# Optimization experiments

Hardware: AMD Instinct MI355X
Metric: run time of the kernel (lower is better)

The kernel has to match this reference:

```python
import jax, jax.numpy as jnp
import numpy as np

B, S, HID, H = 8, 128, 256, 4
DH = HID // H
FF = 4 * HID


def setup_inputs() -> dict:
    key = jax.random.key(0)
    ks = jax.random.split(key, 16)
    n = lambda i, shape: jax.random.normal(ks[i], shape, dtype=jnp.float32) * 0.02
    z = lambda shape: jnp.zeros(shape, dtype=jnp.float32)
    return dict(
        x=jax.random.normal(ks[0], (B, S, HID), dtype=jnp.float32),
        attention_mask=jnp.zeros((B, 1, S, S), dtype=jnp.float32),
        Wq=n(1, (HID, HID)), bq=z((HID,)),
        Wk=n(2, (HID, HID)), bk=z((HID,)),
        Wv=n(3, (HID, HID)), bv=z((HID,)),
        order_w=n(4, (2 * DH,)), order_b=z(()),
        dist_w=n(5, (2 * DH,)), dist_b=z(()),
        scalar=jax.random.normal(ks[6], (1,), dtype=jnp.float32),
        AWq=n(7, (HID, HID)), Abq=z((HID,)),
        AWk=n(8, (HID, HID)), Abk=z((HID,)),
        Wd=n(9, (HID, HID)), bd=z((HID,)),
        g1=jnp.ones((HID,), jnp.float32), beta1=z((HID,)),
        W1=n(10, (HID, FF)), b1=z((FF,)),
        W2=n(11, (FF, HID)), b2=z((HID,)),
        g2=jnp.ones((HID,), jnp.float32), beta2=z((HID,)),
    )


def _ln(t, g, b, eps=1e-12):
    m = t.mean(-1, keepdims=True)
    v = ((t - m) ** 2).mean(-1, keepdims=True)
    return (t - m) / jnp.sqrt(v + eps) * g + b


def _heads(t):
    # [B,S,HID] -> [B,H,S,DH]
    return t.reshape(B, S, H, DH).transpose(0, 2, 1, 3)


def reference(x, attention_mask, Wq, bq, Wk, bk, Wv, bv, order_w, order_b,
              dist_w, dist_b, scalar, AWq, Abq, AWk, Abk, Wd, bd,
              g1, beta1, W1, b1, W2, b2, g2, beta2):
    inv = 1.0 / jnp.sqrt(jnp.float32(DH))
    q = x @ Wq + bq
    k = x @ Wk + bk
    v = x @ Wv + bv
    qh, kh, vh = _heads(q), _heads(k), _heads(v)
    scores = jnp.einsum('bhqd,bhkd->bhqk', qh, kh)  # [B,H,S,S]

    # order/distance affines on concat(q_i, k_j): Linear(2*DH,1) decomposes into
    # per-token projections summed via broadcast (same math, no [B,H,S,S,2*DH] tensor)
    pr_order = jax.nn.sigmoid((qh @ order_w[:DH])[..., :, None]
                              + (kh @ order_w[DH:])[..., None, :] + order_b)
    gd_order = jnp.triu(jnp.ones((S, S), jnp.float32), k=1)
    err_order = (jnp.log(pr_order + 1e-24) * gd_order
                 + jnp.log(1.0 - pr_order + 1e-24) * (1.0 - gd_order))

    idx = jnp.arange(S)
    gd_dist = jnp.log(jnp.abs(idx[None, :] - idx[:, None]).astype(jnp.float32) + 1.0)
    pr_dist = ((qh @ dist_w[:DH])[..., :, None]
               + (kh @ dist_w[DH:])[..., None, :] + dist_b)
    err_dist = -jnp.square(gd_dist - pr_dist) * jnp.square(scalar[0]) * 0.5

    rich_scores = scores + err_order + err_dist
    softm = lambda s: jax.nn.softmax(s * inv + attention_mask, axis=-1)
    rich_probs = softm(rich_scores)
    origin_probs = softm(scores)

    # rich/calibrated combine ('fixed'): softmax(origin + 0.5 * rich)
    combined = jax.nn.softmax(origin_probs + 0.5 * rich_probs, axis=-1)

    # two-level attack attention on transformed mixed q/k
    aq, ak = _heads(q @ AWq + Abq), _heads(k @ AWk + Abk)
    attack_probs = softm(jnp.einsum('bhqd,bhkd->bhqk', aq, ak))
    final_probs = jax.nn.softmax(combined + 0.5 * attack_probs, axis=-1)

    ctx = jnp.einsum('bhqk,bhkd->bhqd', final_probs, vh)
    ctx = ctx.transpose(0, 2, 1, 3).reshape(B, S, HID)
    h = _ln(ctx @ Wd + bd + x, g1, beta1)
    f = jax.nn.gelu(h @ W1 + b1, approximate=False) @ W2 + b2
    return _ln(f + h, g2, beta2)
```

## Files before the change

### kernel.cpp

```cpp
#include <hip/hip_runtime.h>
#include <hip/hip_bf16.h>
#include <math.h>

#define B_  8
#define S_  128
#define HID_ 256
#define H_  4
#define DH_ 64
#define FF_ 1024
#define M_  (B_ * S_)

typedef _Float16 half_t;
typedef __attribute__((ext_vector_type(8))) _Float16 half8;
typedef __attribute__((ext_vector_type(4))) float floatx4;

enum { EP_F32 = 0, EP_F16 = 1, EP_F16B = 2, EP_GELU = 3, EP_PROJ = 4 };

__device__ __forceinline__ floatx4 mfma16(half8 a, half8 b, floatx4 c) {
    return __builtin_amdgcn_mfma_f32_16x16x32_f16(a, b, c, 0, 0, 0);
}

__device__ __forceinline__ float wred_sum(float v) {
#pragma unroll
    for (int o = 32; o >= 1; o >>= 1) v += __shfl_xor(v, o, 64);
    return v;
}
__device__ __forceinline__ float block_sum_256(float v, float* s4, int tid) {
    v = wred_sum(v);
    __syncthreads();
    if ((tid & 63) == 0) s4[tid >> 6] = v;
    __syncthreads();
    return s4[0] + s4[1] + s4[2] + s4[3];
}
__device__ __forceinline__ float qred_sum(float v) {
#pragma unroll
    for (int o = 1; o < 16; o <<= 1) v += __shfl_xor(v, o, 64);
    return v;
}
__device__ __forceinline__ void sm8(float (&v)[8]) {
    float s = 0.f;
#pragma unroll
    for (int j = 0; j < 8; ++j) { v[j] = __expf(v[j]); s += v[j]; }
    s = qred_sum(s);
    float r = 1.f / s;
#pragma unroll
    for (int j = 0; j < 8; ++j) v[j] *= r;
}

template<int EPI>
__device__ __forceinline__ void mgemm(
    const half_t* __restrict__ A, int ldA,
    const half_t* __restrict__ Bt, int ldB,
    int kLen, int m0, int n0,
    const float* __restrict__ bias,
    float* __restrict__ Cf, half_t* __restrict__ Ch, int ldC,
    const float* __restrict__ pw1, const float* __restrict__ pw2,
    float* __restrict__ po1, float* __restrict__ po2, int hsel)
{
    __shared__ half8 Asf[2][4][64];
    __shared__ half8 Bsf[2][4][64];

    const int tid = threadIdx.x;
    const int w = tid >> 6, l = tid & 63;
    const int sr = tid >> 2;
    const int sq = tid & 3;
    const int sdst = (sr & 15) | (sq << 4);
    const int smt = sr >> 4;
    const half_t* Ap = A + (size_t)(m0 + sr) * ldA + sq * 8;
    const half_t* Bp = Bt + (size_t)(n0 + sr) * ldB + sq * 8;

    half8 ra, rb;
    auto fetch = [&](int t) {
        ra = *(const half8*)(Ap + t * 32);
        rb = *(const half8*)(Bp + t * 32);
    };
    auto commit = [&](int buf) {
        Asf[buf][smt][sdst] = ra;
        Bsf[buf][smt][sdst] = rb;
    };

    floatx4 zero = {0.f, 0.f, 0.f, 0.f};
    floatx4 acc[4] = {zero, zero, zero, zero};
    const int kt = kLen >> 5;

    fetch(0);
    commit(0);
    __syncthreads();
    for (int t = 0; t < kt; ++t) {
        const bool more = (t + 1 < kt);
        if (more) fetch(t + 1);
        const int buf = t & 1;
        half8 a = Asf[buf][w][l];
        acc[0] = mfma16(a, Bsf[buf][0][l], acc[0]);
        acc[1] = mfma16(a, Bsf[buf][1][l], acc[1]);
        acc[2] = mfma16(a, Bsf[buf][2][l], acc[2]);
        acc[3] = mfma16(a, Bsf[buf][3][l], acc[3]);
        if (more) {
            commit((t + 1) & 1);
            __syncthreads();
        }
    }

    const int quad = l >> 4, lc = l & 15;
    const int rowb = m0 + w * 16 + quad * 4;
    float bvv[4] = {0.f, 0.f, 0.f, 0.f};
    if (EPI >= EP_F16B) {
#pragma unroll
        for (int nt = 0; nt < 4; ++nt) bvv[nt] = bias[n0 + nt * 16 + lc];
    }
    float pw1v[4], pw2v[4];
    if (EPI == EP_PROJ) {
#pragma unroll
        for (int nt = 0; nt < 4; ++nt) {
            pw1v[nt] = pw1[nt * 16 + lc];
            pw2v[nt] = pw2[nt * 16 + lc];
        }
    }
#pragma unroll
    for (int rr = 0; rr < 4; ++rr) {
        float ov[4];
#pragma unroll
        for (int nt = 0; nt < 4; ++nt) {
            float o = acc[nt][rr];
            if (EPI >= EP_F16B) o += bvv[nt];
            if (EPI == EP_GELU) o = 0.5f * o * (1.f + erff(o * 0.70710678118654752f));
            ov[nt] = o;
            const size_t ci = (size_t)(rowb + rr) * ldC + n0 + nt * 16 + lc;
            if (EPI == EP_F32) Cf[ci] = o;
            else Ch[ci] = (half_t)o;
        }
        if (EPI == EP_PROJ) {
            float po = ov[0] * pw1v[0] + ov[1] * pw1v[1] + ov[2] * pw1v[2] + ov[3] * pw1v[3];
            float pd = ov[0] * pw2v[0] + ov[1] * pw2v[1] + ov[2] * pw2v[2] + ov[3] * pw2v[3];
#pragma unroll
            for (int off = 1; off < 16; off <<= 1) {
                po += __shfl_xor(po, off, 64);
                pd += __shfl_xor(pd, off, 64);
            }
            if (lc == 0) {
                const int m = rowb + rr;
                const int idx = ((m >> 7) * H_ + hsel) * S_ + (m & 127);
                po1[idx] = po;
                po2[idx] = pd;
            }
        }
    }
}

__global__ __launch_bounds__(256) void prep_kernel(
    const float* __restrict__ x,
    const float* __restrict__ Wq, const float* __restrict__ Wk,
    const float* __restrict__ Wv, const float* __restrict__ Wd,
    const float* __restrict__ AWq, const float* __restrict__ AWk,
    const float* __restrict__ W1, const float* __restrict__ W2,
    half_t* __restrict__ x16, half_t* __restrict__ Wq16n, half_t* __restrict__ Wk16n,
    half_t* __restrict__ WqT, half_t* __restrict__ WkT, half_t* __restrict__ WvT,
    half_t* __restrict__ WdT, half_t* __restrict__ AWqT, half_t* __restrict__ AWkT,
    half_t* __restrict__ W1T, half_t* __restrict__ W2T)
{
    const int z = blockIdx.z, bx = blockIdx.x, by = blockIdx.y;
    const int tid = threadIdx.x;
    if (z < 3) {
        const float* src = (z == 0) ? x : (z == 1) ? Wq : Wk;
        half_t* dst = (z == 0) ? x16 : (z == 1) ? Wq16n : Wk16n;
        const int total = (z == 0) ? M_ * HID_ : HID_ * HID_;
        const int bid = by * 16 + bx;
        if (bid * 1024 < total) {
            const int base = bid * 1024 + tid * 4;
            float4 vv = *(const float4*)(src + base);
            dst[base + 0] = (half_t)vv.x;
            dst[base + 1] = (half_t)vv.y;
            dst[base + 2] = (half_t)vv.z;
            dst[base + 3] = (half_t)vv.w;
        }
        return;
    }
    const float* src; half_t* dst; int K, N, k0, n0;
    if (z <= 8) {
        const float* ins[6] = {Wq, Wk, Wv, Wd, AWq, AWk};
        half_t* outs[6] = {WqT, WkT, WvT, WdT, AWqT, AWkT};
        src = ins[z - 3]; dst = outs[z - 3];
        K = 256; N = 256; k0 = bx * 64; n0 = by * 64;
        if (bx >= 4 || by >= 4) return;
    } else if (z == 9) {
        src = W1; dst = W1T; K = 256; N = 1024;
        k0 = bx * 64; n0 = by * 64;
        if (bx >= 4) return;
    } else {
        src = W2; dst = W2T; K = 1024; N = 256;
        k0 = by * 64; n0 = bx * 64;
        if (bx >= 4) return;
    }
    __shared__ half_t tl[64][72];
    const int r = tid >> 2, c0 = (tid & 3) * 16;
#pragma unroll 4
    for (int i = 0; i < 16; ++i)
        tl[c0 + i][r] = (half_t)src[(size_t)(k0 + r) * N + n0 + c0 + i];
    __syncthreads();
#pragma unroll 4
    for (int i = 0; i < 16; ++i)
        dst[(size_t)(n0 + r) * K + k0 + c0 + i] = tl[r][c0 + i];
}

__global__ __launch_bounds__(256) void compose_mfma(
    const half_t* __restrict__ AWqT, const half_t* __restrict__ AWkT,
    const half_t* __restrict__ Wq16n, const half_t* __restrict__ Wk16n,
    const float* __restrict__ AWq, const float* __restrict__ AWk,
    const float* __restrict__ bq, const float* __restrict__ bk,
    const float* __restrict__ Abq, const float* __restrict__ Abk,
    half_t* __restrict__ WcqT, half_t* __restrict__ WckT,
    float* __restrict__ bcq, float* __restrict__ bck)
{
    const int z = blockIdx.z;
    if (blockIdx.y < 4) {
        const half_t* A = z ? AWkT : AWqT;
        const half_t* Bt = z ? Wk16n : Wq16n;
        half_t* C = z ? WckT : WcqT;
        mgemm<EP_F16>(A, HID_, Bt, HID_, HID_, blockIdx.y * 64, blockIdx.x * 64,
                      nullptr, nullptr, C, HID_, nullptr, nullptr, nullptr, nullptr, 0);
    } else {
        __shared__ float red[4][64];
        const float* bsrc = z ? bk : bq;
        const float* AW   = z ? AWk : AWq;
        const float* Ab   = z ? Abk : Abq;
        float* bco        = z ? bck : bcq;
        int t = threadIdx.x, l = t & 63, kc = t >> 6;
        int n = blockIdx.x * 64 + l;
        float p = 0.f;
#pragma unroll 8
        for (int kk = 0; kk < 64; ++kk) {
            int k = kc * 64 + kk;
            p = fmaf(bsrc[k], AW[(size_t)k * HID_ + n], p);
        }
        red[kc][l] = p;
        __syncthreads();
        if (kc == 0)
            bco[n] = red[0][l] + red[1][l] + red[2][l] + red[3][l] + Ab[n];
    }
}

__global__ __launch_bounds__(256) void xgemm5(
    const half_t* __restrict__ x16,
    const half_t* __restrict__ WqT, const float* __restrict__ bq,
    const half_t* __restrict__ WkT, const float* __restrict__ bk,
    const half_t* __restrict__ WvT, const float* __restrict__ bv,
    const half_t* __restrict__ WcqT, const float* __restrict__ bcq,
    const half_t* __restrict__ WckT, const float* __restrict__ bck,
    const float* __restrict__ order_w, const float* __restrict__ dist_w,
    half_t* __restrict__ q16, half_t* __restrict__ k16, half_t* __restrict__ v16,
    half_t* __restrict__ aq16, half_t* __restrict__ ak16,
    float* __restrict__ qoA, float* __restrict__ qdA,
    float* __restrict__ koA, float* __restrict__ kdA)
{
    const int z = blockIdx.z;
    const int m0 = blockIdx.y * 64, n0 = blockIdx.x * 64;
    if (z == 0)
        mgemm<EP_PROJ>(x16, HID_, WqT, HID_, HID_, m0, n0, bq, nullptr, q16, HID_,
                       order_w, dist_w, qoA, qdA, blockIdx.x);
    else if (z == 1)
        mgemm<EP_PROJ>(x16, HID_, WkT, HID_, HID_, m0, n0, bk, nullptr, k16, HID_,
                       order_w + DH_, dist_w + DH_, koA, kdA, blockIdx.x);
    else if (z == 2)
        mgemm<EP_F16B>(x16, HID_, WvT, HID_, HID_, m0, n0, bv, nullptr, v16, HID_,
                       nullptr, nullptr, nullptr, nullptr, 0);
    else if (z == 3)
        mgemm<EP_F16B>(x16, HID_, WcqT, HID_, HID_, m0, n0, bcq, nullptr, aq16, HID_,
                       nullptr, nullptr, nullptr, nullptr, 0);
    else
        mgemm<EP_F16B>(x16, HID_, WckT, HID_, HID_, m0, n0, bck, nullptr, ak16, HID_,
                       nullptr, nullptr, nullptr, nullptr, 0);
}

__global__ __launch_bounds__(64) void attn_fused(
    const half_t* __restrict__ q16, const half_t* __restrict__ k16,
    const half_t* __restrict__ v16, const half_t* __restrict__ aq16,
    const half_t* __restrict__ ak16,
    const float* __restrict__ qoA, const float* __restrict__ qdA,
    const float* __restrict__ koA, const float* __restrict__ kdA,
    const float* __restrict__ mask,
    const float* __restrict__ order_b_p, const float* __restrict__ dist_b_p,
    const float* __restrict__ scalar_p,
    half_t* __restrict__ ctx16)
{
    __shared__ half8 Qf[2][64], AQf[2][64];
    __shared__ half8 Kf[2][8][64], AKf[2][8][64];
    __shared__ half_t Vt[64][136];
    __shared__ half_t Pm[16][136];

    const int l = threadIdx.x;
    const int quad = l >> 4, lc = l & 15;
    const int bh = blockIdx.x >> 3, rt = blockIdx.x & 7;
    const int b = bh >> 2, h = bh & 3;
    const size_t hoff = (size_t)b * S_ * HID_ + h * DH_;

#pragma unroll
    for (int u = 0; u < 2; ++u) {
        int idx = u * 64 + l;
        int r = idx >> 3, c = idx & 7;
        size_t g = hoff + (size_t)(rt * 16 + r) * HID_ + c * 8;
        int kt = c >> 2, sl = r | ((c & 3) << 4);
        Qf[kt][sl]  = *(const half8*)(q16 + g);
        AQf[kt][sl] = *(const half8*)(aq16 + g);
    }
#pragma unroll
    for (int u = 0; u < 16; ++u) {
        int idx = u * 64 + l;
        int j = idx >> 3, c = idx & 7;
        size_t g = hoff + (size_t)j * HID_ + c * 8;
        int kt = c >> 2, jt = j >> 4, sl = (j & 15) | ((c & 3) << 4);
        Kf[kt][jt][sl]  = *(const half8*)(k16 + g);
        AKf[kt][jt][sl] = *(const half8*)(ak16 + g);
    }
#pragma unroll
    for (int u = 0; u < 16; ++u) {
        int j = (u >> 3) * 64 + l;
        int c = u & 7;
        half8 vv = *(const half8*)(v16 + hoff + (size_t)j * HID_ + c * 8);
#pragma unroll
        for (int e = 0; e < 8; ++e) Vt[c * 8 + e][j] = vv[e];
    }
    __syncthreads();

    floatx4 zero = {0.f, 0.f, 0.f, 0.f};
    floatx4 accS[8], accA[8];
#pragma unroll
    for (int jt = 0; jt < 8; ++jt) { accS[jt] = zero; accA[jt] = zero; }
#pragma unroll
    for (int kt = 0; kt < 2; ++kt) {
        half8 a0 = Qf[kt][l];
        half8 a1 = AQf[kt][l];
#pragma unroll
        for (int jt = 0; jt < 8; ++jt) {
            accS[jt] = mfma16(a0, Kf[kt][jt][l], accS[jt]);
            accA[jt] = mfma16(a1, AKf[kt][jt][l], accA[jt]);
        }
    }

    const float ob = order_b_p[0], db = dist_b_p[0];
    const float scl = scalar_p[0];
    const float s2 = scl * scl;
    const float inv = 0.125f;
    float kov[8], kdv[8];
#pragma unroll
    for (int jt = 0; jt < 8; ++jt) {
        kov[jt] = koA[bh * S_ + jt * 16 + lc];
        kdv[jt] = kdA[bh * S_ + jt * 16 + lc];
    }
#pragma unroll
    for (int reg = 0; reg < 4; ++reg) {
        const int il = quad * 4 + reg;
        const int i  = rt * 16 + il;
        float qo = qoA[bh * S_ + i], qd = qdA[bh * S_ + i];
        const float* mrow = mask + ((size_t)(b * S_ + i)) * S_;
        float mk[8], lg[8], as_[8];
#pragma unroll
        for (int jt = 0; jt < 8; ++jt) {
            mk[jt] = mrow[jt * 16 + lc];
            lg[jt] = accS[jt][reg];
            as_[jt] = accA[jt][reg];
        }
        float p0[8];
#pragma unroll
        for (int jt = 0; jt < 8; ++jt) p0[jt] = lg[jt] * inv + mk[jt];
        sm8(p0);
        float p1[8];
#pragma unroll
        for (int jt = 0; jt < 8; ++jt) {
            int j = jt * 16 + lc;
            float pr = 1.f / (1.f + __expf(-(qo + kov[jt] + ob)));
            float sel = (j > i) ? pr : 1.f - pr;
            float erro = __logf(sel + 1e-24f);
            float gd = __logf(fabsf((float)(j - i)) + 1.f);
            float dd = gd - (qd + kdv[jt] + db);
            p1[jt] = (lg[jt] + erro - 0.5f * dd * dd * s2) * inv + mk[jt];
        }
        sm8(p1);
#pragma unroll
        for (int jt = 0; jt < 8; ++jt) p0[jt] += 0.5f * p1[jt];
        sm8(p0);
#pragma unroll
        for (int jt = 0; jt < 8; ++jt) p1[jt] = as_[jt] * inv + mk[jt];
        sm8(p1);
#pragma unroll
        for (int jt = 0; jt < 8; ++jt) p0[jt] += 0.5f * p1[jt];
        sm8(p0);
#pragma unroll
        for (int jt = 0; jt < 8; ++jt) Pm[il][jt * 16 + lc] = (half_t)p0[jt];
    }
    __syncthreads();

    half8 pa_[4];
#pragma unroll
    for (int kt = 0; kt < 4; ++kt)
        pa_[kt] = *(const half8*)&Pm[lc][kt * 32 + quad * 8];
    floatx4 apv[4];
#pragma unroll
    for (int nt = 0; nt < 4; ++nt) apv[nt] = zero;
#pragma unroll
    for (int nt = 0; nt < 4; ++nt) {
#pragma unroll
        for (int kt = 0; kt < 4; ++kt) {
            half8 vf = *(const half8*)&Vt[nt * 16 + lc][kt * 32 + quad * 8];
            apv[nt] = mfma16(pa_[kt], vf, apv[nt]);
        }
    }
#pragma unroll
    for (int nt = 0; nt < 4; ++nt) {
#pragma unroll
        for (int reg = 0; reg < 4; ++reg) {
            int i = rt * 16 + quad * 4 + reg;
            ctx16[hoff + (size_t)i * HID_ + nt * 16 + lc] = (half_t)apv[nt][reg];
        }
    }
}

__global__ __launch_bounds__(256) void dense_mfma(
    const half_t* __restrict__ ctx16, const half_t* __restrict__ WdT,
    float* __restrict__ dn)
{
    mgemm<EP_F32>(ctx16, HID_, WdT, HID_, HID_, blockIdx.y * 64, blockIdx.x * 64,
                  nullptr, dn, nullptr, HID_, nullptr, nullptr, nullptr, nullptr, 0);
}

__global__ __launch_bounds__(256) void ff1_mfma(
    const half_t* __restrict__ h16, const half_t* __restrict__ W1T,
    const float* __restrict__ b1, half_t* __restrict__ f116)
{
    mgemm<EP_GELU>(h16, HID_, W1T, HID_, HID_, blockIdx.y * 64, blockIdx.x * 64,
                   b1, nullptr, f116, FF_, nullptr, nullptr, nullptr, nullptr, 0);
}

__global__ __launch_bounds__(256) void ff2_mfma(
    const half_t* __restrict__ f116, const half_t* __restrict__ W2T,
    float* __restrict__ p0, float* __restrict__ p1,
    float* __restrict__ p2, float* __restrict__ p3)
{
    const int z = blockIdx.z;
    float* C = (z == 0) ? p0 : (z == 1) ? p1 : (z == 2) ? p2 : p3;
    mgemm<EP_F32>(f116 + z * 256, FF_, W2T + z * 256, FF_, 256,
                  blockIdx.y * 64, blockIdx.x * 64,
                  nullptr, C, nullptr, HID_, nullptr, nullptr, nullptr, nullptr, 0);
}

__global__ __launch_bounds__(256) void ln1_kernel(
    const float* __restrict__ dn, const float* __restrict__ bd,
    const float* __restrict__ x,
    const float* __restrict__ g1, const float* __restrict__ beta1,
    float* __restrict__ h32, half_t* __restrict__ h16)
{
    __shared__ float s4[4];
    const int row = blockIdx.x;
    const int n = threadIdx.x;
    const size_t idx = (size_t)row * HID_ + n;
    float val = dn[idx] + bd[n] + x[idx];
    float mean = block_sum_256(val, s4, n) * (1.f / HID_);
    float dv = val - mean;
    float var = block_sum_256(dv * dv, s4, n) * (1.f / HID_);
    float r = dv * rsqrtf(var + 1e-12f) * g1[n] + beta1[n];
    h32[idx] = r;
    h16[idx] = (half_t)r;
}

__global__ __launch_bounds__(256) void ln2_kernel(
    const float* __restrict__ p0, const float* __restrict__ p1,
    const float* __restrict__ p2, const float* __restrict__ p3,
    const float* __restrict__ b2, const float* __restrict__ h32,
    const float* __restrict__ g2, const float* __restrict__ beta2,
    float* __restrict__ out)
{
    __shared__ float s4[4];
    const int row = blockIdx.x;
    const int n = threadIdx.x;
    const size_t idx = (size_t)row * HID_ + n;
    float val = p0[idx] + p1[idx] + p2[idx] + p3[idx] + b2[n] + h32[idx];
    float mean = block_sum_256(val, s4, n) * (1.f / HID_);
    float dv = val - mean;
    float var = block_sum_256(dv * dv, s4, n) * (1.f / HID_);
    out[idx] = dv * rsqrtf(var + 1e-12f) * g2[n] + beta2[n];
}

extern "C" void kernel_launch(void* const* d_in, const int* in_sizes, int n_in,
                              void* d_out, int out_size, void* d_ws, size_t ws_size,
                              hipStream_t stream) {
    const float* x        = (const float*)d_in[0];
    const float* mask     = (const float*)d_in[1];
    const float* Wq       = (const float*)d_in[2];
    const float* bq       = (const float*)d_in[3];
    const float* Wk       = (const float*)d_in[4];
    const float* bk       = (const float*)d_in[5];
    const float* Wv       = (const float*)d_in[6];
    const float* bv       = (const float*)d_in[7];
    const float* order_w  = (const float*)d_in[8];
    const float* order_b  = (const float*)d_in[9];
    const float* dist_w   = (const float*)d_in[10];
    const float* dist_b   = (const float*)d_in[11];
    const float* scalar   = (const float*)d_in[12];
    const float* AWq      = (const float*)d_in[13];
    const float* Abq      = (const float*)d_in[14];
    const float* AWk      = (const float*)d_in[15];
    const float* Abk      = (const float*)d_in[16];
    const float* Wd       = (const float*)d_in[17];
    const float* bd       = (const float*)d_in[18];
    const float* g1       = (const float*)d_in[19];
    const float* beta1    = (const float*)d_in[20];
    const float* W1       = (const float*)d_in[21];
    const float* b1       = (const float*)d_in[22];
    const float* W2       = (const float*)d_in[23];
    const float* b2       = (const float*)d_in[24];
    const float* g2       = (const float*)d_in[25];
    const float* beta2    = (const float*)d_in[26];

    float* ws = (float*)d_ws;
    size_t off = 0;
    auto afl = [&](size_t n) { float* p = ws + off; off += n; return p; };
    auto ahf = [&](size_t nh) { half_t* p = (half_t*)(ws + off); off += nh / 2; return p; };

    half_t* x16   = ahf(M_ * HID_);
    half_t* Wq16n = ahf(HID_ * HID_);
    half_t* Wk16n = ahf(HID_ * HID_);
    half_t* WqT   = ahf(HID_ * HID_);
    half_t* WkT   = ahf(HID_ * HID_);
    half_t* WvT   = ahf(HID_ * HID_);
    half_t* WdT   = ahf(HID_ * HID_);
    half_t* AWqT  = ahf(HID_ * HID_);
    half_t* AWkT  = ahf(HID_ * HID_);
    half_t* W1T   = ahf(HID_ * FF_);
    half_t* W2T   = ahf(HID_ * FF_);
    half_t* WcqT  = ahf(HID_ * HID_);
    half_t* WckT  = ahf(HID_ * HID_);
    half_t* q16   = ahf(M_ * HID_);
    half_t* k16   = ahf(M_ * HID_);
    half_t* v16   = ahf(M_ * HID_);
    half_t* aq16  = ahf(M_ * HID_);
    half_t* ak16  = ahf(M_ * HID_);
    half_t* ctx16 = ahf(M_ * HID_);
    half_t* h16   = ahf(M_ * HID_);
    half_t* f116  = ahf(M_ * FF_);
    float* dnb  = afl(M_ * HID_);
    float* hb32 = afl(M_ * HID_);
    float* pf0  = afl(M_ * HID_);
    float* pf1  = afl(M_ * HID_);
    float* pf2  = afl(M_ * HID_);
    float* pf3  = afl(M_ * HID_);
    float* bcq  = afl(256);
    float* bck  = afl(256);
    float* qoA  = afl(B_ * H_ * S_);
    float* qdA  = afl(B_ * H_ * S_);
    float* koA  = afl(B_ * H_ * S_);
    float* kdA  = afl(B_ * H_ * S_);

    prep_kernel<<<dim3(16, 16, 11), 256, 0, stream>>>(
        x, Wq, Wk, Wv, Wd, AWq, AWk, W1, W2,
        x16, Wq16n, Wk16n, WqT, WkT, WvT, WdT, AWqT, AWkT, W1T, W2T);
    compose_mfma<<<dim3(4, 5, 2), 256, 0, stream>>>(
        AWqT, AWkT, Wq16n, Wk16n, AWq, AWk, bq, bk, Abq, Abk, WcqT, WckT, bcq, bck);
    xgemm5<<<dim3(4, 16, 5), 256, 0, stream>>>(
        x16, WqT, bq, WkT, bk, WvT, bv, WcqT, bcq, WckT, bck, order_w, dist_w,
        q16, k16, v16, aq16, ak16, qoA, qdA, koA, kdA);
    attn_fused<<<256, 64, 0, stream>>>(
        q16, k16, v16, aq16, ak16, qoA, qdA, koA, kdA,
        mask, order_b, dist_b, scalar, ctx16);
    dense_mfma<<<dim3(4, 16), 256, 0, stream>>>(ctx16, WdT, dnb);
    ln1_kernel<<<M_, 256, 0, stream>>>(dnb, bd, x, g1, beta1, hb32, h16);
    ff1_mfma<<<dim3(16, 16), 256, 0, stream>>>(h16, W1T, b1, f116);
    ff2_mfma<<<dim3(4, 16, 4), 256, 0, stream>>>(f116, W2T, pf0, pf1, pf2, pf3);
    ln2_kernel<<<M_, 256, 0, stream>>>(pf0, pf1, pf2, pf3, b2, hb32, g2, beta2, (float*)d_out);
}
```

Before: 162.7 us.

## Fuse all stages into one cooperative persistent kernel with grid syncs

Replaces the chain of nine kernel launches with a single cooperative kernel of 256 blocks that runs each stage as jobs separated by grid-wide barriers. It also fuses the dense projection with LayerNorm1, and FF2 with LayerNorm2, using 16-row tiles, which removes the split-K partial buffers and the separate LN kernels. The aim is to remove launch overhead and inter-kernel gaps on a small, latency-bound workload. The cost is grid-sync overhead, a larger shared-memory union that may limit occupancy, and fewer active blocks in the fused dense and FF2 stages. The old multi-kernel path is kept as a fallback if the cooperative launch fails.

New measurement: 390.7 us. 140% more time.

```diff
diff --git a/kernel.cpp b/kernel.cpp
--- a/kernel.cpp
+++ b/kernel.cpp
@@ -1,6 +1,8 @@
 #include <hip/hip_runtime.h>
-#include <hip/hip_bf16.h>
+#include <hip/hip_cooperative_groups.h>
 #include <math.h>
+
+namespace cg = cooperative_groups;
 
 #define B_  8
 #define S_  128
@@ -49,6 +51,7 @@
 
 template<int EPI>
 __device__ __forceinline__ void mgemm(
+    half8 (&Asf)[2][4][64], half8 (&Bsf)[2][4][64],
     const half_t* __restrict__ A, int ldA,
     const half_t* __restrict__ Bt, int ldB,
     int kLen, int m0, int n0,
@@ -57,9 +60,6 @@
     const float* __restrict__ pw1, const float* __restrict__ pw2,
     float* __restrict__ po1, float* __restrict__ po2, int hsel)
 {
-    __shared__ half8 Asf[2][4][64];
-    __shared__ half8 Bsf[2][4][64];
-
     const int tid = threadIdx.x;
     const int w = tid >> 6, l = tid & 63;
     const int sr = tid >> 2;
@@ -146,6 +146,374 @@
         }
     }
 }
+
+
+struct MegaParams {
+    const float *x, *mask, *Wq, *bq, *Wk, *bk, *Wv, *bv;
+    const float *order_w, *order_b, *dist_w, *dist_b, *scalar;
+    const float *AWq, *Abq, *AWk, *Abk, *Wd, *bd, *g1, *beta1;
+    const float *W1, *b1, *W2, *b2, *g2, *beta2;
+    half_t *x16, *Wq16n, *Wk16n, *WqT, *WkT, *WvT, *WdT, *AWqT, *AWkT, *W1T, *W2T;
+    half_t *WcqT, *WckT;
+    half_t *q16, *k16, *v16, *aq16, *ak16, *ctx16, *h16, *f116;
+    float *hb32, *bcq, *bck, *qoA, *qdA, *koA, *kdA;
+    float *out;
+};
+
+union SMem {
+    struct { half8 Asf[2][4][64]; half8 Bsf[2][4][64]; } g;
+    struct { half_t tl[64][72]; } p;
+    struct { float red[4][64]; } r;
+    struct {
+        half8 Kf[2][8][64]; half8 AKf[2][8][64];
+        half_t Vt[64][136]; half_t Pm[16][136];
+    } a;
+    struct { half8 Af[8][64]; float hS[16][257]; } d;
+    struct { half8 Af2[32][64]; float hS[16][257]; } f;
+};
+
+#define NJOBS_PREP 608
+__device__ __forceinline__ void prep_job(const MegaParams& P, SMem& sm, int j, int tid) {
+    if (j < 384) {
+        const float* src; half_t* dst; int base;
+        if (j < 256)      { src = P.x;  dst = P.x16;   base = j * 1024; }
+        else if (j < 320) { src = P.Wq; dst = P.Wq16n; base = (j - 256) * 1024; }
+        else              { src = P.Wk; dst = P.Wk16n; base = (j - 320) * 1024; }
+        float4 vv = *(const float4*)(src + base + tid * 4);
+        dst[base + tid * 4 + 0] = (half_t)vv.x;
+        dst[base + tid * 4 + 1] = (half_t)vv.y;
+        dst[base + tid * 4 + 2] = (half_t)vv.z;
+        dst[base + tid * 4 + 3] = (half_t)vv.w;
+        return;
+    }
+    int t = j - 384;
+    const float* src; half_t* dst; int K, N, k0, n0;
+    if (t < 96) {
+        int m = t >> 4, q = t & 15;
+        const float* ins[6] = {P.Wq, P.Wk, P.Wv, P.Wd, P.AWq, P.AWk};
+        half_t* outs[6] = {P.WqT, P.WkT, P.WvT, P.WdT, P.AWqT, P.AWkT};
+        src = ins[m]; dst = outs[m]; K = 256; N = 256;
+        k0 = (q & 3) * 64; n0 = (q >> 2) * 64;
+    } else if (t < 160) {
+        int q = t - 96; src = P.W1; dst = P.W1T; K = 256; N = 1024;
+        k0 = (q & 3) * 64; n0 = (q >> 2) * 64;
+    } else {
+        int q = t - 160; src = P.W2; dst = P.W2T; K = 1024; N = 256;
+        k0 = (q >> 2) * 64; n0 = (q & 3) * 64;
+    }
+    __syncthreads();
+    const int r = tid >> 2, c0 = (tid & 3) * 16;
+#pragma unroll 4
+    for (int i = 0; i < 16; ++i)
+        sm.p.tl[c0 + i][r] = (half_t)src[(size_t)(k0 + r) * N + n0 + c0 + i];
+    __syncthreads();
+#pragma unroll 4
+    for (int i = 0; i < 16; ++i)
+        dst[(size_t)(n0 + r) * K + k0 + c0 + i] = sm.p.tl[r][c0 + i];
+}
+
+__device__ __forceinline__ void compose_job(const MegaParams& P, SMem& sm, int blk, int tid) {
+    if (blk < 32) {
+        int z = blk >> 4, q = blk & 15;
+        const half_t* A  = z ? P.AWkT : P.AWqT;
+        const half_t* Bt = z ? P.Wk16n : P.Wq16n;
+        half_t* C = z ? P.WckT : P.WcqT;
+        mgemm<EP_F16>(sm.g.Asf, sm.g.Bsf, A, HID_, Bt, HID_, HID_,
+                      (q >> 2) * 64, (q & 3) * 64,
+                      nullptr, nullptr, C, HID_, nullptr, nullptr, nullptr, nullptr, 0);
+    } else {
+        int q = blk - 32;
+        int z = q >> 2, xb = q & 3;
+        const float* bsrc = z ? P.bk : P.bq;
+        const float* AW   = z ? P.AWk : P.AWq;
+        const float* Ab   = z ? P.Abk : P.Abq;
+        float* bco        = z ? P.bck : P.bcq;
+        int l = tid & 63, kc = tid >> 6;
+        int n = xb * 64 + l;
+        float p = 0.f;
+#pragma unroll 8
+        for (int kk = 0; kk < 64; ++kk) {
+            int k = kc * 64 + kk;
+            p = fmaf(bsrc[k], AW[(size_t)k * HID_ + n], p);
+        }
+        sm.r.red[kc][l] = p;
+        __syncthreads();
+        if (kc == 0)
+            bco[n] = sm.r.red[0][l] + sm.r.red[1][l] + sm.r.red[2][l] + sm.r.red[3][l] + Ab[n];
+    }
+}
+
+__device__ __forceinline__ void xgemm_job(const MegaParams& P, SMem& sm, int j) {
+    const int z = j >> 6, q = j & 63;
+    const int m0 = (q >> 2) * 64, n0 = (q & 3) * 64, bx = q & 3;
+    if (z == 0)
+        mgemm<EP_PROJ>(sm.g.Asf, sm.g.Bsf, P.x16, HID_, P.WqT, HID_, HID_, m0, n0,
+                       P.bq, nullptr, P.q16, HID_, P.order_w, P.dist_w, P.qoA, P.qdA, bx);
+    else if (z == 1)
+        mgemm<EP_PROJ>(sm.g.Asf, sm.g.Bsf, P.x16, HID_, P.WkT, HID_, HID_, m0, n0,
+                       P.bk, nullptr, P.k16, HID_, P.order_w + DH_, P.dist_w + DH_, P.koA, P.kdA, bx);
+    else if (z == 2)
+        mgemm<EP_F16B>(sm.g.Asf, sm.g.Bsf, P.x16, HID_, P.WvT, HID_, HID_, m0, n0,
+                       P.bv, nullptr, P.v16, HID_, nullptr, nullptr, nullptr, nullptr, 0);
+    else if (z == 3)
+        mgemm<EP_F16B>(sm.g.Asf, sm.g.Bsf, P.x16, HID_, P.WcqT, HID_, HID_, m0, n0,
+                       P.bcq, nullptr, P.aq16, HID_, nullptr, nullptr, nullptr, nullptr, 0);
+    else
+        mgemm<EP_F16B>(sm.g.Asf, sm.g.Bsf, P.x16, HID_, P.WckT, HID_, HID_, m0, n0,
+                       P.bck, nullptr, P.ak16, HID_, nullptr, nullptr, nullptr, nullptr, 0);
+}
+
+__device__ __forceinline__ void attn_job(const MegaParams& P, SMem& sm, int blk, int tid) {
+    const int bh = blk >> 3, rt = blk & 7;
+    const int b = bh >> 2, h = bh & 3;
+    const size_t hoff = (size_t)b * S_ * HID_ + (size_t)h * DH_;
+    const int l = tid & 63, w = tid >> 6;
+    const int quad = l >> 4, lc = l & 15;
+
+#pragma unroll
+    for (int u = 0; u < 4; ++u) {
+        int idx = u * 256 + tid;
+        int j = idx >> 3, c = idx & 7;
+        size_t g = hoff + (size_t)j * HID_ + c * 8;
+        int kt = c >> 2, jt = j >> 4, sl = (j & 15) | ((c & 3) << 4);
+        sm.a.Kf[kt][jt][sl]  = *(const half8*)(P.k16 + g);
+        sm.a.AKf[kt][jt][sl] = *(const half8*)(P.ak16 + g);
+    }
+#pragma unroll
+    for (int u = 0; u < 4; ++u) {
+        int idx = u * 256 + tid;
+        int j = idx >> 3, c = idx & 7;
+        half8 vv = *(const half8*)(P.v16 + hoff + (size_t)j * HID_ + c * 8);
+#pragma unroll
+        for (int e = 0; e < 8; ++e) sm.a.Vt[c * 8 + e][j] = vv[e];
+    }
+    __syncthreads();
+
+    if (w == 0) {
+        half8 qf[2], aqf[2];
+#pragma unroll
+        for (int kt = 0; kt < 2; ++kt) {
+            size_t g = hoff + (size_t)(rt * 16 + lc) * HID_ + kt * 32 + quad * 8;
+            qf[kt]  = *(const half8*)(P.q16 + g);
+            aqf[kt] = *(const half8*)(P.aq16 + g);
+        }
+        floatx4 zero = {0.f, 0.f, 0.f, 0.f};
+        floatx4 accS[8], accA[8];
+#pragma unroll
+        for (int jt = 0; jt < 8; ++jt) { accS[jt] = zero; accA[jt] = zero; }
+#pragma unroll
+        for (int kt = 0; kt < 2; ++kt) {
+#pragma unroll
+            for (int jt = 0; jt < 8; ++jt) {
+                accS[jt] = mfma16(qf[kt], sm.a.Kf[kt][jt][l], accS[jt]);
+                accA[jt] = mfma16(aqf[kt], sm.a.AKf[kt][jt][l], accA[jt]);
+            }
+        }
+
+        const float ob = P.order_b[0], db = P.dist_b[0];
+        const float scl = P.scalar[0];
+        const float s2 = scl * scl;
+        const float inv = 0.125f;
+        float kov[8], kdv[8];
+#pragma unroll
+        for (int jt = 0; jt < 8; ++jt) {
+            kov[jt] = P.koA[bh * S_ + jt * 16 + lc];
+            kdv[jt] = P.kdA[bh * S_ + jt * 16 + lc];
+        }
+#pragma unroll
+        for (int reg = 0; reg < 4; ++reg) {
+            const int il = quad * 4 + reg;
+            const int i  = rt * 16 + il;
+            float qo = P.qoA[bh * S_ + i], qd = P.qdA[bh * S_ + i];
+            const float* mrow = P.mask + ((size_t)(b * S_ + i)) * S_;
+            float mk[8], lg[8], as_[8];
+#pragma unroll
+            for (int jt = 0; jt < 8; ++jt) {
+                mk[jt] = mrow[jt * 16 + lc];
+                lg[jt] = accS[jt][reg];
+                as_[jt] = accA[jt][reg];
+            }
+            float p0[8];
+#pragma unroll
+            for (int jt = 0; jt < 8; ++jt) p0[jt] = lg[jt] * inv + mk[jt];
+            sm8(p0);
+            float p1[8];
+#pragma unroll
+            for (int jt = 0; jt < 8; ++jt) {
+                int j = jt * 16 + lc;
+                float pr = 1.f / (1.f + __expf(-(qo + kov[jt] + ob)));
+                float sel = (j > i) ? pr : 1.f - pr;
+                float erro = __logf(sel + 1e-24f);
+                float gd = __logf(fabsf((float)(j - i)) + 1.f);
+                float dd = gd - (qd + kdv[jt] + db);
+                p1[jt] = (lg[jt] + erro - 0.5f * dd * dd * s2) * inv + mk[jt];
+            }
+            sm8(p1);
+#pragma unroll
+            for (int jt = 0; jt < 8; ++jt) p0[jt] += 0.5f * p1[jt];
+            sm8(p0);
+#pragma unroll
+            for (int jt = 0; jt < 8; ++jt) p1[jt] = as_[jt] * inv + mk[jt];
+            sm8(p1);
+#pragma unroll
+            for (int jt = 0; jt < 8; ++jt) p0[jt] += 0.5f * p1[jt];
+            sm8(p0);
+#pragma unroll
+            for (int jt = 0; jt < 8; ++jt) sm.a.Pm[il][jt * 16 + lc] = (half_t)p0[jt];
+        }
+    }
+    __syncthreads();
+
+    if (w == 0) {
+        half8 pa_[4];
+#pragma unroll
+        for (int kt = 0; kt < 4; ++kt)
+            pa_[kt] = *(const half8*)&sm.a.Pm[lc][kt * 32 + quad * 8];
+        floatx4 zero = {0.f, 0.f, 0.f, 0.f};
+        floatx4 apv[4] = {zero, zero, zero, zero};
+#pragma unroll
+        for (int nt = 0; nt < 4; ++nt) {
+#pragma unroll
+            for (int kt = 0; kt < 4; ++kt) {
+                half8 vf = *(const half8*)&sm.a.Vt[nt * 16 + lc][kt * 32 + quad * 8];
+                apv[nt] = mfma16(pa_[kt], vf, apv[nt]);
+            }
+        }
+#pragma unroll
+        for (int nt = 0; nt < 4; ++nt) {
+#pragma unroll
+            for (int reg = 0; reg < 4; ++reg) {
+                int i = rt * 16 + quad * 4 + reg;
+                P.ctx16[hoff + (size_t)i * HID_ + nt * 16 + lc] = (half_t)apv[nt][reg];
+            }
+        }
+    }
+}
+
+template<bool DUAL>
+__device__ __forceinline__ void ln16(float (&hS)[16][257], int tid, int r0,
+    const float* __restrict__ g, const float* __restrict__ be,
+    float* __restrict__ o32, half_t* __restrict__ o16, float* __restrict__ oo) {
+    const int row = tid >> 4, jj = tid & 15;
+    float s = 0.f;
+#pragma unroll
+    for (int i = 0; i < 16; ++i) s += hS[row][i * 16 + jj];
+#pragma unroll
+    for (int o = 1; o < 16; o <<= 1) s += __shfl_xor(s, o, 64);
+    const float mean = s * (1.f / 256.f);
+    float vs = 0.f;
+#pragma unroll
+    for (int i = 0; i < 16; ++i) { float d = hS[row][i * 16 + jj] - mean; vs += d * d; }
+#pragma unroll
+    for (int o = 1; o < 16; o <<= 1) vs += __shfl_xor(vs, o, 64);
+    const float rs = rsqrtf(vs * (1.f / 256.f) + 1e-12f);
+#pragma unroll
+    for (int i = 0; i < 16; ++i) {
+        int col = i * 16 + jj;
+        float v = (hS[row][col] - mean) * rs * g[col] + be[col];
+        size_t gi = (size_t)(r0 + row) * HID_ + col;
+        if (DUAL) { o32[gi] = v; o16[gi] = (half_t)v; }
+        else      { oo[gi] = v; }
+    }
+}
+
+__device__ __forceinline__ void dense_ln1_job(const MegaParams& P, SMem& sm, int blk, int tid) {
+    const int r0 = blk * 16;
+#pragma unroll
+    for (int u = 0; u < 2; ++u) {
+        int idx = u * 256 + tid;
+        int row = idx >> 5, c = idx & 31;
+        sm.d.Af[c >> 2][row | ((c & 3) << 4)] =
+            *(const half8*)(P.ctx16 + (size_t)(r0 + row) * HID_ + c * 8);
+    }
+    __syncthreads();
+    const int w = tid >> 6, l = tid & 63;
+    const int n0 = w * 64, quad = l >> 4, lc = l & 15;
+    floatx4 zero = {0.f, 0.f, 0.f, 0.f};
+    floatx4 acc[4] = {zero, zero, zero, zero};
+#pragma unroll
+    for (int kt = 0; kt < 8; ++kt) {
+        half8 a = sm.d.Af[kt][l];
+#pragma unroll
+        for (int nt = 0; nt < 4; ++nt) {
+            half8 b = *(const half8*)(P.WdT + (size_t)(n0 + nt * 16 + lc) * HID_ + kt * 32 + quad * 8);
+            acc[nt] = mfma16(a, b, acc[nt]);
+        }
+    }
+#pragma unroll
+    for (int nt = 0; nt < 4; ++nt) {
+#pragma unroll
+        for (int rr = 0; rr < 4; ++rr) {
+            int row = quad * 4 + rr, col = n0 + nt * 16 + lc;
+            sm.d.hS[row][col] = acc[nt][rr] + P.bd[col] + P.x[(size_t)(r0 + row) * HID_ + col];
+        }
+    }
+    __syncthreads();
+    ln16<true>(sm.d.hS, tid, r0, P.g1, P.beta1, P.hb32, P.h16, nullptr);
+}
+
+__device__ __forceinline__ void ff1_job(const MegaParams& P, SMem& sm, int blk) {
+    mgemm<EP_GELU>(sm.g.Asf, sm.g.Bsf, P.h16, HID_, P.W1T, HID_, HID_,
+                   (blk >> 4) * 64, (blk & 15) * 64,
+                   P.b1, nullptr, P.f116, FF_, nullptr, nullptr, nullptr, nullptr, 0);
+}
+
+__device__ __forceinline__ void ff2_ln2_job(const MegaParams& P, SMem& sm, int blk, int tid) {
+    const int r0 = blk * 16;
+#pragma unroll
+    for (int u = 0; u < 8; ++u) {
+        int idx = u * 256 + tid;
+        int row = idx >> 7, c = idx & 127;
+        sm.f.Af2[c >> 2][row | ((c & 3) << 4)] =
+            *(const half8*)(P.f116 + (size_t)(r0 + row) * FF_ + c * 8);
+    }
+    __syncthreads();
+    const int w = tid >> 6, l = tid & 63;
+    const int n0 = w * 64, quad = l >> 4, lc = l & 15;
+    floatx4 zero = {0.f, 0.f, 0.f, 0.f};
+    floatx4 acc[4] = {zero, zero, zero, zero};
+#pragma unroll
+    for (int kt = 0; kt < 32; ++kt) {
+        half8 a = sm.f.Af2[kt][l];
+#pragma unroll
+        for (int nt = 0; nt < 4; ++nt) {
+            half8 b = *(const half8*)(P.W2T + (size_t)(n0 + nt * 16 + lc) * FF_ + kt * 32 + quad * 8);
+            acc[nt] = mfma16(a, b, acc[nt]);
+        }
+    }
+#pragma unroll
+    for (int nt = 0; nt < 4; ++nt) {
+#pragma unroll
+        for (int rr = 0; rr < 4; ++rr) {
+            int row = quad * 4 + rr, col = n0 + nt * 16 + lc;
+            sm.f.hS[row][col] = acc[nt][rr] + P.b2[col] + P.hb32[(size_t)(r0 + row) * HID_ + col];
+        }
+    }
+    __syncthreads();
+    ln16<false>(sm.f.hS, tid, r0, P.g2, P.beta2, nullptr, nullptr, P.out);
+}
+
+__global__ __launch_bounds__(256) void mega_kernel(MegaParams P) {
+    cg::grid_group gg = cg::this_grid();
+    __shared__ SMem sm;
+    const int blk = blockIdx.x, tid = threadIdx.x;
+
+    for (int j = blk; j < NJOBS_PREP; j += 256) prep_job(P, sm, j, tid);
+    __syncthreads(); gg.sync();
+    if (blk < 40) compose_job(P, sm, blk, tid);
+    __syncthreads(); gg.sync();
+    xgemm_job(P, sm, blk);
+    if (blk < 64) { __syncthreads(); xgemm_job(P, sm, blk + 256); }
+    __syncthreads(); gg.sync();
+    attn_job(P, sm, blk, tid);
+    __syncthreads(); gg.sync();
+    if (blk < 64) dense_ln1_job(P, sm, blk, tid);
+    __syncthreads(); gg.sync();
+    ff1_job(P, sm, blk);
+    __syncthreads(); gg.sync();
+    if (blk < 64) ff2_ln2_job(P, sm, blk, tid);
+}
+
 
 __global__ __launch_bounds__(256) void prep_kernel(
     const float* __restrict__ x,
@@ -211,12 +579,13 @@
     half_t* __restrict__ WcqT, half_t* __restrict__ WckT,
     float* __restrict__ bcq, float* __restrict__ bck)
 {
+    __shared__ half8 As[2][4][64], Bs[2][4][64];
     const int z = blockIdx.z;
     if (blockIdx.y < 4) {
         const half_t* A = z ? AWkT : AWqT;
         const half_t* Bt = z ? Wk16n : Wq16n;
         half_t* C = z ? WckT : WcqT;
-        mgemm<EP_F16>(A, HID_, Bt, HID_, HID_, blockIdx.y * 64, blockIdx.x * 64,
+        mgemm<EP_F16>(As, Bs, A, HID_, Bt, HID_, HID_, blockIdx.y * 64, blockIdx.x * 64,
                       nullptr, nullptr, C, HID_, nullptr, nullptr, nullptr, nullptr, 0);
     } else {
         __shared__ float red[4][64];
@@ -252,22 +621,23 @@
     float* __restrict__ qoA, float* __restrict__ qdA,
     float* __restrict__ koA, float* __restrict__ kdA)
 {
+    __shared__ half8 As[2][4][64], Bs[2][4][64];
     const int z = blockIdx.z;
     const int m0 = blockIdx.y * 64, n0 = blockIdx.x * 64;
     if (z == 0)
-        mgemm<EP_PROJ>(x16, HID_, WqT, HID_, HID_, m0, n0, bq, nullptr, q16, HID_,
+        mgemm<EP_PROJ>(As, Bs, x16, HID_, WqT, HID_, HID_, m0, n0, bq, nullptr, q16, HID_,
                        order_w, dist_w, qoA, qdA, blockIdx.x);
     else if (z == 1)
-        mgemm<EP_PROJ>(x16, HID_, WkT, HID_, HID_, m0, n0, bk, nullptr, k16, HID_,
+        mgemm<EP_PROJ>(As, Bs, x16, HID_, WkT, HID_, HID_, m0, n0, bk, nullptr, k16, HID_,
                        order_w + DH_, dist_w + DH_, koA, kdA, blockIdx.x);
     else if (z == 2)
-        mgemm<EP_F16B>(x16, HID_, WvT, HID_, HID_, m0, n0, bv, nullptr, v16, HID_,
+        mgemm<EP_F16B>(As, Bs, x16, HID_, WvT, HID_, HID_, m0, n0, bv, nullptr, v16, HID_,
                        nullptr, nullptr, nullptr, nullptr, 0);
     else if (z == 3)
-        mgemm<EP_F16B>(x16, HID_, WcqT, HID_, HID_, m0, n0, bcq, nullptr, aq16, HID_,
+        mgemm<EP_F16B>(As, Bs, x16, HID_, WcqT, HID_, HID_, m0, n0, bcq, nullptr, aq16, HID_,
                        nullptr, nullptr, nullptr, nullptr, 0);
     else
-        mgemm<EP_F16B>(x16, HID_, WckT, HID_, HID_, m0, n0, bck, nullptr, ak16, HID_,
+        mgemm<EP_F16B>(As, Bs, x16, HID_, WckT, HID_, HID_, m0, n0, bck, nullptr, ak16, HID_,
                        nullptr, nullptr, nullptr, nullptr, 0);
 }
 
@@ -418,7 +788,8 @@
     const half_t* __restrict__ ctx16, const half_t* __restrict__ WdT,
     float* __restrict__ dn)
 {
-    mgemm<EP_F32>(ctx16, HID_, WdT, HID_, HID_, blockIdx.y * 64, blockIdx.x * 64,
+    __shared__ half8 As[2][4][64], Bs[2][4][64];
+    mgemm<EP_F32>(As, Bs, ctx16, HID_, WdT, HID_, HID_, blockIdx.y * 64, blockIdx.x * 64,
                   nullptr, dn, nullptr, HID_, nullptr, nullptr, nullptr, nullptr, 0);
 }
 
@@ -426,7 +797,8 @@
     const half_t* __restrict__ h16, const half_t* __restrict__ W1T,
     const float* __restrict__ b1, half_t* __restrict__ f116)
 {
-    mgemm<EP_GELU>(h16, HID_, W1T, HID_, HID_, blockIdx.y * 64, blockIdx.x * 64,
+    __shared__ half8 As[2][4][64], Bs[2][4][64];
+    mgemm<EP_GELU>(As, Bs, h16, HID_, W1T, HID_, HID_, blockIdx.y * 64, blockIdx.x * 64,
                    b1, nullptr, f116, FF_, nullptr, nullptr, nullptr, nullptr, 0);
 }
 
@@ -435,9 +807,10 @@
     float* __restrict__ p0, float* __restrict__ p1,
     float* __restrict__ p2, float* __restrict__ p3)
 {
+    __shared__ half8 As[2][4][64], Bs[2][4][64];
     const int z = blockIdx.z;
     float* C = (z == 0) ? p0 : (z == 1) ? p1 : (z == 2) ? p2 : p3;
-    mgemm<EP_F32>(f116 + z * 256, FF_, W2T + z * 256, FF_, 256,
+    mgemm<EP_F32>(As, Bs, f116 + z * 256, FF_, W2T + z * 256, FF_, 256,
                   blockIdx.y * 64, blockIdx.x * 64,
                   nullptr, C, nullptr, HID_, nullptr, nullptr, nullptr, nullptr, 0);
 }
@@ -549,20 +922,43 @@
     float* koA  = afl(B_ * H_ * S_);
     float* kdA  = afl(B_ * H_ * S_);
 
-    prep_kernel<<<dim3(16, 16, 11), 256, 0, stream>>>(
-        x, Wq, Wk, Wv, Wd, AWq, AWk, W1, W2,
-        x16, Wq16n, Wk16n, WqT, WkT, WvT, WdT, AWqT, AWkT, W1T, W2T);
-    compose_mfma<<<dim3(4, 5, 2), 256, 0, stream>>>(
-        AWqT, AWkT, Wq16n, Wk16n, AWq, AWk, bq, bk, Abq, Abk, WcqT, WckT, bcq, bck);
-    xgemm5<<<dim3(4, 16, 5), 256, 0, stream>>>(
-        x16, WqT, bq, WkT, bk, WvT, bv, WcqT, bcq, WckT, bck, order_w, dist_w,
-        q16, k16, v16, aq16, ak16, qoA, qdA, koA, kdA);
-    attn_fused<<<256, 64, 0, stream>>>(
-        q16, k16, v16, aq16, ak16, qoA, qdA, koA, kdA,
-        mask, order_b, dist_b, scalar, ctx16);
-    dense_mfma<<<dim3(4, 16), 256, 0, stream>>>(ctx16, WdT, dnb);
-    ln1_kernel<<<M_, 256, 0, stream>>>(dnb, bd, x, g1, beta1, hb32, h16);
-    ff1_mfma<<<dim3(16, 16), 256, 0, stream>>>(h16, W1T, b1, f116);
-    ff2_mfma<<<dim3(4, 16, 4), 256, 0, stream>>>(f116, W2T, pf0, pf1, pf2, pf3);
-    ln2_kernel<<<M_, 256, 0, stream>>>(pf0, pf1, pf2, pf3, b2, hb32, g2, beta2, (float*)d_out);
-}
+    MegaParams mp;
+    mp.x = x; mp.mask = mask; mp.Wq = Wq; mp.bq = bq; mp.Wk = Wk; mp.bk = bk;
+    mp.Wv = Wv; mp.bv = bv; mp.order_w = order_w; mp.order_b = order_b;
+    mp.dist_w = dist_w; mp.dist_b = dist_b; mp.scalar = scalar;
+    mp.AWq = AWq; mp.Abq = Abq; mp.AWk = AWk; mp.Abk = Abk;
+    mp.Wd = Wd; mp.bd = bd; mp.g1 = g1; mp.beta1 = beta1;
+    mp.W1 = W1; mp.b1 = b1; mp.W2 = W2; mp.b2 = b2; mp.g2 = g2; mp.beta2 = beta2;
+    mp.x16 = x16; mp.Wq16n = Wq16n; mp.Wk16n = Wk16n;
+    mp.WqT = WqT; mp.WkT = WkT; mp.WvT = WvT; mp.WdT = WdT;
+    mp.AWqT = AWqT; mp.AWkT = AWkT; mp.W1T = W1T; mp.W2T = W2T;
+    mp.WcqT = WcqT; mp.WckT = WckT;
+    mp.q16 = q16; mp.k16 = k16; mp.v16 = v16; mp.aq16 = aq16; mp.ak16 = ak16;
+    mp.ctx16 = ctx16; mp.h16 = h16; mp.f116 = f116;
+    mp.hb32 = hb32; mp.bcq = bcq; mp.bck = bck;
+    mp.qoA = qoA; mp.qdA = qdA; mp.koA = koA; mp.kdA = kdA;
+    mp.out = (float*)d_out;
+
+    void* kargs[] = { (void*)&mp };
+    hipError_t e = hipLaunchCooperativeKernel((const void*)mega_kernel,
+                                              dim3(256), dim3(256), kargs, 0, stream);
+    if (e != hipSuccess) {
+        (void)hipGetLastError();
+        prep_kernel<<<dim3(16, 16, 11), 256, 0, stream>>>(
+            x, Wq, Wk, Wv, Wd, AWq, AWk, W1, W2,
+            x16, Wq16n, Wk16n, WqT, WkT, WvT, WdT, AWqT, AWkT, W1T, W2T);
+        compose_mfma<<<dim3(4, 5, 2), 256, 0, stream>>>(
+            AWqT, AWkT, Wq16n, Wk16n, AWq, AWk, bq, bk, Abq, Abk, WcqT, WckT, bcq, bck);
+        xgemm5<<<dim3(4, 16, 5), 256, 0, stream>>>(
+            x16, WqT, bq, WkT, bk, WvT, bv, WcqT, bcq, WckT, bck, order_w, dist_w,
+            q16, k16, v16, aq16, ak16, qoA, qdA, koA, kdA);
+        attn_fused<<<256, 64, 0, stream>>>(
+            q16, k16, v16, aq16, ak16, qoA, qdA, koA, kdA,
+            mask, order_b, dist_b, scalar, ctx16);
+        dense_mfma<<<dim3(4, 16), 256, 0, stream>>>(ctx16, WdT, dnb);
+        ln1_kernel<<<M_, 256, 0, stream>>>(dnb, bd, x, g1, beta1, hb32, h16);
+        ff1_mfma<<<dim3(16, 16), 256, 0, stream>>>(h16, W1T, b1, f116);
+        ff2_mfma<<<dim3(4, 16, 4), 256, 0, stream>>>(f116, W2T, pf0, pf1, pf2, pf3);
+        ln2_kernel<<<M_, 256, 0, stream>>>(pf0, pf1, pf2, pf3, b2, hb32, g2, beta2, (float*)d_out);
+    }
+}
```
